# Performance work log

Hardware: AMD Instinct MI355X
Metric: run time of the kernel (lower is better)

The kernel has to match this reference:

```python
import jax, jax.numpy as jnp
import numpy as np

D_IN = 1024
D_OUT = 1024
NUM_HEADS = 16
HEAD_DIM = D_OUT // NUM_HEADS
CONTEXT_LEN = 2048


def setup_inputs() -> dict:
    key = jax.random.key(0)
    ks = jax.random.split(key, 7)
    scale = 0.02
    x = jax.random.normal(ks[0], (2, 2048, D_IN), dtype=jnp.float32)
    Wq = jax.random.normal(ks[1], (D_IN, D_OUT), dtype=jnp.float32) * scale
    bq = jnp.zeros((D_OUT,), dtype=jnp.float32)
    Wk = jax.random.normal(ks[2], (D_IN, D_OUT), dtype=jnp.float32) * scale
    bk = jnp.zeros((D_OUT,), dtype=jnp.float32)
    Wv = jax.random.normal(ks[3], (D_IN, D_OUT), dtype=jnp.float32) * scale
    bv = jnp.zeros((D_OUT,), dtype=jnp.float32)
    return {"x": x, "Wq": Wq, "bq": bq, "Wk": Wk, "bk": bk, "Wv": Wv, "bv": bv}


def reference(x, Wq, bq, Wk, bk, Wv, bv):
    B, S, _ = x.shape
    # QKV projections with bias
    q = x @ Wq + bq  # [B,S,D_OUT]
    k = x @ Wk + bk
    v = x @ Wv + bv
    # split heads -> [B,H,S,Dh]
    def heads(t):
        return t.reshape(B, S, NUM_HEADS, HEAD_DIM).transpose(0, 2, 1, 3)
    q, k, v = heads(q), heads(k), heads(v)
    # raw scores, then additive causal mask (-1e9 on strictly upper triangle),
    # then scale by 1/sqrt(head_dim) AFTER adding mask (matches original code)
    scores = jnp.einsum("bhqd,bhkd->bhqk", q, k)
    causal = jnp.tril(jnp.ones((S, S), dtype=bool))
    add_mask = jnp.where(causal, 0.0, -1e9).astype(scores.dtype)
    scores = scores + add_mask
    weights = jax.nn.softmax(scores / jnp.sqrt(jnp.asarray(HEAD_DIM, scores.dtype)), axis=-1)
    ctx = jnp.einsum("bhqk,bhkd->bhqd", weights, v)  # [B,H,S,Dh]
    return ctx.transpose(0, 2, 1, 3).reshape(B, S, D_OUT)
```

## Files before the change

### kernel.cpp

```cpp
#include <hip/hip_runtime.h>
#include <hip/hip_bf16.h>
#include <stdint.h>

#define D_IN 1024
#define NH 16
#define DH 64
#define SEQ 2048
#define BATCH 2

typedef unsigned short u16;
typedef __attribute__((ext_vector_type(8))) short short8;
typedef __attribute__((ext_vector_type(4))) float f32x4;

#define CSCALE 0.1803368801f

__device__ __forceinline__ u16 f2bf(float f) {
    union { float f; uint32_t u; } v; v.f = f;
    uint32_t r = v.u + 0x7FFF + ((v.u >> 16) & 1);
    return (u16)(r >> 16);
}

__device__ __forceinline__ float bf2f(u16 u) {
    union { uint32_t u; float f; } v; v.u = (uint32_t)u << 16;
    return v.f;
}

__device__ __forceinline__ uint32_t pktrunc(float a, float b) {
    union { float f; uint32_t u; } x, y;
    x.f = a; y.f = b;
    return __builtin_amdgcn_perm(y.u, x.u, 0x07060302u);
}

__device__ __forceinline__ void async16(const u16* g, u16* l) {
    __builtin_amdgcn_global_load_lds(
        (const __attribute__((address_space(1))) void*)g,
        (__attribute__((address_space(3))) void*)l, 16, 0, 0);
}

__global__ __launch_bounds__(256) void prep_kernel(
    const float* __restrict__ x, const float* __restrict__ Wq,
    const float* __restrict__ Wk, const float* __restrict__ Wv,
    u16* __restrict__ xb, u16* __restrict__ WT)
{
    __shared__ float tile[64][65];
    if (blockIdx.x < 4096) {
        int i = (blockIdx.x * 256 + threadIdx.x) * 4;
        float4 v = *(const float4*)(x + i);
        union { u16 u[4]; uint2 d; } o;
        o.u[0] = f2bf(v.x); o.u[1] = f2bf(v.y); o.u[2] = f2bf(v.z); o.u[3] = f2bf(v.w);
        *(uint2*)(xb + i) = o.d;
        return;
    }
    int idx = blockIdx.x - 4096;
    int mat = idx >> 8, rem = idx & 255;
    int k0 = (rem & 15) * 64, n0 = (rem >> 4) * 64;
    const float* W = (mat == 0) ? Wq : (mat == 1 ? Wk : Wv);
    int c = threadIdx.x & 63, rb = threadIdx.x >> 6;
    #pragma unroll
    for (int p = 0; p < 16; ++p) {
        int r = p * 4 + rb;
        tile[r][c] = W[(size_t)(k0 + r) * 1024 + n0 + c];
    }
    __syncthreads();
    #pragma unroll
    for (int p = 0; p < 16; ++p) {
        int r = p * 4 + rb;
        WT[((size_t)mat * 1024 + n0 + r) * 1024 + k0 + c] = f2bf(tile[c][r]);
    }
}

__global__ __launch_bounds__(512, 2) void qkv_gemm_kernel(
    const u16* __restrict__ xb, const u16* __restrict__ WT,
    const float* __restrict__ bq, const float* __restrict__ bk,
    const float* __restrict__ bv,
    u16* __restrict__ Qb, u16* __restrict__ Kb, u16* __restrict__ Vt)
{
    __shared__ u16 smem[65536];
    u16* As = smem;
    u16* Bs = smem + 32768;

    const int tid  = threadIdx.x;
    const int wave = tid >> 6, lane = tid & 63;
    const int quad = lane >> 4, l15 = lane & 15;
    const int wm = wave >> 2, wn = wave & 3;
    const int fsig = l15 & 7;

    const int lin = blockIdx.x;
    const int logical = (lin & 7) * 24 + (lin >> 3);
    const int by = logical / 12;
    const int bx = logical % 12;
    const int m0 = by * 256;
    const int n0 = bx * 256;

    const int ch  = tid & 7;
    const int rwT = tid >> 3;

    f32x4 acc[8][4];
    #pragma unroll
    for (int i = 0; i < 8; ++i)
        #pragma unroll
        for (int j = 0; j < 4; ++j)
            acc[i][j] = (f32x4){0.f, 0.f, 0.f, 0.f};

    auto stageA = [&](int buf, int kst) {
        #pragma unroll
        for (int r = 0; r < 4; ++r) {
            int row = r * 64 + rwT;
            int g = ch ^ (row & 7);
            async16(xb + (size_t)(m0 + row) * 1024 + kst + g * 8,
                    As + buf * 16384 + row * 64 + ch * 8);
        }
    };
    auto stageBh = [&](int buf, int kst, int half) {
        #pragma unroll
        for (int r = 0; r < 2; ++r) {
            int row = half * 128 + r * 64 + rwT;
            int g = ch ^ (row & 7);
            async16(WT + (size_t)(n0 + row) * 1024 + kst + g * 8,
                    Bs + buf * 16384 + row * 64 + ch * 8);
        }
    };

    stageA(0, 0);  stageBh(0, 0, 0);  stageBh(0, 0, 1);
    stageA(1, 64); stageBh(1, 64, 0); stageBh(1, 64, 1);
    asm volatile("s_waitcnt vmcnt(8)" ::: "memory");
    __builtin_amdgcn_sched_barrier(0);
    __builtin_amdgcn_s_barrier();

    for (int t = 0; t < 16; ++t) {
        const int cur = t & 1;
        const u16* Ab = As + cur * 16384;
        const u16* Bb = Bs + cur * 16384;
        const bool st = (t + 2 < 16);
        const int k2 = (t + 2) * 64;

        short8 bfr[4][2];
        #pragma unroll
        for (int j = 0; j < 4; ++j)
            #pragma unroll
            for (int kk = 0; kk < 2; ++kk)
                bfr[j][kk] = *(const short8*)(Bb + (wn * 64 + j * 16 + l15) * 64 +
                                              (((kk << 2) + quad) ^ fsig) * 8);

        #pragma unroll
        for (int p = 0; p < 4; ++p) {
            short8 af[2][2];
            #pragma unroll
            for (int i2 = 0; i2 < 2; ++i2)
                #pragma unroll
                for (int kk = 0; kk < 2; ++kk)
                    af[i2][kk] = *(const short8*)(Ab + (wm * 128 + (p * 2 + i2) * 16 + l15) * 64 +
                                                  (((kk << 2) + quad) ^ fsig) * 8);
            if (p == 1 && st) stageBh(cur, k2, 0);
            if (p == 2 && st) stageBh(cur, k2, 1);
            __builtin_amdgcn_s_barrier();
            if (p == 3 && st) stageA(cur, k2);
            __builtin_amdgcn_s_setprio(1);
            #pragma unroll
            for (int kk = 0; kk < 2; ++kk)
                #pragma unroll
                for (int i2 = 0; i2 < 2; ++i2)
                    #pragma unroll
                    for (int j = 0; j < 4; ++j)
                        acc[p * 2 + i2][j] = __builtin_amdgcn_mfma_f32_16x16x32_bf16(
                            af[i2][kk], bfr[j][kk], acc[p * 2 + i2][j], 0, 0, 0);
            __builtin_amdgcn_s_setprio(0);
            if (p == 3) {
                if (st)            { asm volatile("s_waitcnt vmcnt(8)" ::: "memory"); }
                else if (t == 14)  { asm volatile("s_waitcnt vmcnt(0)" ::: "memory"); }
                __builtin_amdgcn_sched_barrier(0);
            }
            __builtin_amdgcn_s_barrier();
        }
    }
    __syncthreads();

    const int mat = n0 >> 10;
    const int ncb = (n0 & 1023) + wn * 64;
    const int hh = ncb >> 6;
    const int bb = m0 >> 11, sb = m0 & 2047;

    if (mat < 2) {
        const float* bias = (mat == 0) ? bq : bk;
        u16* dst = (mat == 0) ? Qb : Kb;
        const float sc = (mat == 0) ? CSCALE : 1.0f;
        #pragma unroll
        for (int i = 0; i < 8; ++i) {
            int ss = sb + wm * 128 + i * 16 + quad * 4;
            #pragma unroll
            for (int j = 0; j < 4; ++j) {
                int dh = j * 16 + l15;
                float bval = bias[ncb + dh];
                size_t base = (((size_t)bb * NH + hh) * SEQ + ss) * DH + dh;
                #pragma unroll
                for (int r = 0; r < 4; ++r)
                    dst[base + (size_t)r * DH] = f2bf((acc[i][j][r] + bval) * sc);
            }
        }
    } else {
        u16* vt = smem + wave * (64 * 72);
        u16* vdst = Vt + ((size_t)(bb * NH + hh) * DH) * SEQ;
        #pragma unroll
        for (int h2 = 0; h2 < 2; ++h2) {
            #pragma unroll
            for (int i = 0; i < 4; ++i)
                #pragma unroll
                for (int j = 0; j < 4; ++j) {
                    float bval = bv[ncb + j * 16 + l15];
                    union { u16 u[4]; uint2 d; } o;
                    #pragma unroll
                    for (int r = 0; r < 4; ++r)
                        o.u[r] = f2bf(acc[h2 * 4 + i][j][r] + bval);
                    *(uint2*)(vt + (j * 16 + l15) * 72 + i * 16 + quad * 4) = o.d;
                }
            const int s0w = sb + wm * 128 + h2 * 64;
            #pragma unroll
            for (int it = 0; it < 8; ++it) {
                int dh = it * 8 + (lane >> 3);
                short8 v = *(const short8*)(vt + dh * 72 + (lane & 7) * 8);
                *(short8*)(vdst + (size_t)dh * SEQ + s0w + (lane & 7) * 8) = v;
            }
        }
    }
}

__device__ __forceinline__ void stage64(const u16* g0, size_t gstride, u16* lds,
                                        int wave, int lane)
{
    #pragma unroll
    for (int rnd = 0; rnd < 2; ++rnd) {
        int row = rnd * 32 + wave * 8 + (lane >> 3);
        int sig = ((row >> 3) & 1) * 4 + (row & 3);
        int c = (lane & 7) ^ sig;
        async16(g0 + (size_t)row * gstride + c * 8, lds + row * 64 + (lane & 7) * 8);
    }
}

__global__ __launch_bounds__(256) void flash_mfma_kernel(
    const u16* __restrict__ Qb, const u16* __restrict__ Kb,
    const u16* __restrict__ Vt, float* __restrict__ out,
    u16* __restrict__ Opart, float* __restrict__ Lpart)
{
    static const int JQT[24] = {7,15,15,14,14, 6,13,13,12,12, 5,11,11,10,10,
                                4, 9, 9, 8, 8, 3, 2, 1, 0};
    static const int JHF[24] = {-1,0,1,0,1, -1,0,1,0,1, -1,0,1,0,1,
                                -1,0,1,0,1, -1,-1,-1,-1};

    __shared__ u16 Ks[2][64 * 64];
    __shared__ u16 Vs[2][64 * 64];

    const int tid  = threadIdx.x;
    const int wave = tid >> 6, lane = tid & 63;
    const int quad = lane >> 4, l15 = lane & 15;
    const int bhx = blockIdx.x;
    const int b = bhx >> 4, h = bhx & 15;
    const int job = blockIdx.y;
    const int qt = JQT[job], hf = JHF[job];
    const int t0 = (hf == 1) ? qt + 1 : 0;
    const int t1 = (hf == 0) ? qt + 1 : 2 * qt + 2;
    const int q0 = qt * 128;
    const int wq0 = wave * 32;
    const size_t bh = (size_t)bhx;
    const u16* Qp = Qb + bh * SEQ * DH;
    const u16* Kp = Kb + bh * SEQ * DH;
    const u16* Vp = Vt + bh * DH * SEQ;

    short8 qf[2][2];
    #pragma unroll
    for (int qa = 0; qa < 2; ++qa) {
        const u16* qrp = Qp + (size_t)(q0 + wq0 + qa * 16 + l15) * DH;
        qf[qa][0] = *(const short8*)(qrp + quad * 8);
        qf[qa][1] = *(const short8*)(qrp + 32 + quad * 8);
    }

    const short8 ones = (short8){0x3F80, 0x3F80, 0x3F80, 0x3F80,
                                 0x3F80, 0x3F80, 0x3F80, 0x3F80};

    f32x4 O[2][4], L[2];
    #pragma unroll
    for (int pa = 0; pa < 2; ++pa) {
        #pragma unroll
        for (int f = 0; f < 4; ++f) O[pa][f] = (f32x4){0.f, 0.f, 0.f, 0.f};
        L[pa] = (f32x4){0.f, 0.f, 0.f, 0.f};
    }

    const int wqmax = q0 + wq0 + 31;
    const int krbase = (l15 >> 2) * 8 + (l15 & 3);
    const int ksig   = ((l15 >> 2) & 1) * 4 + (l15 & 3);
    const int vsig   = ((l15 >> 3) & 1) * 4 + (l15 & 3);

    stage64(Kp + (size_t)t0 * 64 * DH, DH, Ks[t0 & 1], wave, lane);
    stage64(Vp + t0 * 64, SEQ, Vs[t0 & 1], wave, lane);
    __syncthreads();

    for (int t = t0; t < t1; ++t) {
        const int cur = t & 1;
        if (t + 1 < t1) {
            int k1 = (t + 1) * 64;
            stage64(Kp + (size_t)k1 * DH, DH, Ks[cur ^ 1], wave, lane);
            stage64(Vp + k1, SEQ, Vs[cur ^ 1], wave, lane);
        }
        const int k0 = t * 64;
        if (k0 <= wqmax) {
            f32x4 sf[4][2];
            #pragma unroll
            for (int fj = 0; fj < 4; ++fj) {
                int krow = (fj >> 1) * 32 + krbase + (fj & 1) * 4;
                const u16* kp = &Ks[cur][krow * 64];
                short8 k0f = *(const short8*)(kp + (quad ^ ksig) * 8);
                short8 k1f = *(const short8*)(kp + ((4 + quad) ^ ksig) * 8);
                #pragma unroll
                for (int qa = 0; qa < 2; ++qa) {
                    f32x4 s = (f32x4){0.f, 0.f, 0.f, 0.f};
                    s = __builtin_amdgcn_mfma_f32_16x16x32_bf16(k0f, qf[qa][0], s, 0, 0, 0);
                    s = __builtin_amdgcn_mfma_f32_16x16x32_bf16(k1f, qf[qa][1], s, 0, 0, 0);
                    sf[fj][qa] = s;
                }
            }
            const bool diag = (k0 + 63 > q0 + wq0);
            short8 pA[2][2];
            #pragma unroll
            for (int qa = 0; qa < 2; ++qa) {
                #pragma unroll
                for (int fj = 0; fj < 4; ++fj)
                    #pragma unroll
                    for (int r = 0; r < 4; ++r) {
                        float p = __builtin_amdgcn_exp2f(sf[fj][qa][r]);
                        if (diag) {
                            int key = k0 + (fj >> 1) * 32 + quad * 8 + (fj & 1) * 4 + r;
                            int qg  = q0 + wq0 + qa * 16 + l15;
                            p = (key <= qg) ? p : 0.f;
                        }
                        sf[fj][qa][r] = p;
                    }
                union { uint32_t d[4]; short8 v; } a0, a1;
                a0.d[0] = pktrunc(sf[0][qa][0], sf[0][qa][1]);
                a0.d[1] = pktrunc(sf[0][qa][2], sf[0][qa][3]);
                a0.d[2] = pktrunc(sf[1][qa][0], sf[1][qa][1]);
                a0.d[3] = pktrunc(sf[1][qa][2], sf[1][qa][3]);
                a1.d[0] = pktrunc(sf[2][qa][0], sf[2][qa][1]);
                a1.d[1] = pktrunc(sf[2][qa][2], sf[2][qa][3]);
                a1.d[2] = pktrunc(sf[3][qa][0], sf[3][qa][1]);
                a1.d[3] = pktrunc(sf[3][qa][2], sf[3][qa][3]);
                pA[qa][0] = a0.v;
                pA[qa][1] = a1.v;
                L[qa] = __builtin_amdgcn_mfma_f32_16x16x32_bf16(pA[qa][0], ones, L[qa], 0, 0, 0);
                L[qa] = __builtin_amdgcn_mfma_f32_16x16x32_bf16(pA[qa][1], ones, L[qa], 0, 0, 0);
            }
            #pragma unroll
            for (int fo = 0; fo < 4; ++fo) {
                const u16* vrow = &Vs[cur][(fo * 16 + l15) * 64];
                short8 vb0 = *(const short8*)(vrow + (quad ^ vsig) * 8);
                short8 vb1 = *(const short8*)(vrow + ((4 + quad) ^ vsig) * 8);
                #pragma unroll
                for (int pa = 0; pa < 2; ++pa) {
                    O[pa][fo] = __builtin_amdgcn_mfma_f32_16x16x32_bf16(pA[pa][0], vb0, O[pa][fo], 0, 0, 0);
                    O[pa][fo] = __builtin_amdgcn_mfma_f32_16x16x32_bf16(pA[pa][1], vb1, O[pa][fo], 0, 0, 0);
                }
            }
        }
        __syncthreads();
    }

    if (hf < 0) {
        #pragma unroll
        for (int pa = 0; pa < 2; ++pa)
            #pragma unroll
            for (int fo = 0; fo < 4; ++fo)
                #pragma unroll
                for (int r = 0; r < 4; ++r) {
                    int s = q0 + wq0 + pa * 16 + quad * 4 + r;
                    out[((size_t)b * SEQ + s) * 1024 + h * DH + fo * 16 + l15] =
                        O[pa][fo][r] / L[pa][r];
                }
    } else {
        const int pi = (qt - 8) * 2 + hf;
        u16* op = Opart + (((size_t)pi * 32 + bhx) * 128) * 64;
        float* lp = Lpart + ((size_t)pi * 32 + bhx) * 128;
        #pragma unroll
        for (int pa = 0; pa < 2; ++pa) {
            #pragma unroll
            for (int fo = 0; fo < 4; ++fo)
                #pragma unroll
                for (int r = 0; r < 4; ++r) {
                    int ql = wq0 + pa * 16 + quad * 4 + r;
                    op[(size_t)ql * 64 + fo * 16 + l15] = f2bf(O[pa][fo][r]);
                }
            if (l15 == 0) {
                #pragma unroll
                for (int r = 0; r < 4; ++r)
                    lp[wq0 + pa * 16 + quad * 4 + r] = L[pa][r];
            }
        }
    }
}

__global__ __launch_bounds__(256) void combine_kernel(
    const u16* __restrict__ Opart, const float* __restrict__ Lpart,
    float* __restrict__ out)
{
    int blk = blockIdx.x;
    int qt = 8 + (blk >> 5);
    int bh = blk & 31;
    int b = bh >> 4, h = bh & 15;
    int pi0 = (qt - 8) * 2, pi1 = pi0 + 1;
    int tid = threadIdx.x;
    int q = tid >> 1, seg = (tid & 1) * 32;
    const u16* o0 = Opart + (((size_t)pi0 * 32 + bh) * 128 + q) * 64 + seg;
    const u16* o1 = Opart + (((size_t)pi1 * 32 + bh) * 128 + q) * 64 + seg;
    float inv = 1.0f / (Lpart[((size_t)pi0 * 32 + bh) * 128 + q] +
                        Lpart[((size_t)pi1 * 32 + bh) * 128 + q]);
    float* op = out + ((size_t)b * SEQ + qt * 128 + q) * 1024 + h * DH + seg;
    #pragma unroll
    for (int d = 0; d < 32; d += 4) {
        union { uint2 d2; u16 u[4]; } a, c;
        a.d2 = *(const uint2*)(o0 + d);
        c.d2 = *(const uint2*)(o1 + d);
        float4 v;
        v.x = (bf2f(a.u[0]) + bf2f(c.u[0])) * inv;
        v.y = (bf2f(a.u[1]) + bf2f(c.u[1])) * inv;
        v.z = (bf2f(a.u[2]) + bf2f(c.u[2])) * inv;
        v.w = (bf2f(a.u[3]) + bf2f(c.u[3])) * inv;
        *(float4*)(op + d) = v;
    }
}

extern "C" void kernel_launch(void* const* d_in, const int* in_sizes, int n_in,
                              void* d_out, int out_size, void* d_ws, size_t ws_size,
                              hipStream_t stream) {
    const float* x  = (const float*)d_in[0];
    const float* Wq = (const float*)d_in[1];
    const float* bq = (const float*)d_in[2];
    const float* Wk = (const float*)d_in[3];
    const float* bk = (const float*)d_in[4];
    const float* Wv = (const float*)d_in[5];
    const float* bv = (const float*)d_in[6];
    float* out = (float*)d_out;

    const size_t NX = (size_t)BATCH * SEQ * D_IN;
    const size_t NW = (size_t)3 * D_IN * 1024;
    const size_t NP = (size_t)BATCH * NH * SEQ * DH;
    u16* xb = (u16*)d_ws;
    u16* WT = xb + NX;
    u16* Qb = WT + NW;
    u16* Kb = Qb + NP;
    u16* Vt = Kb + NP;
    u16* Opart = xb;
    float* Lpart = (float*)(xb + NX);

    prep_kernel<<<4096 + 768, 256, 0, stream>>>(x, Wq, Wk, Wv, xb, WT);
    qkv_gemm_kernel<<<dim3(192), 512, 0, stream>>>(xb, WT, bq, bk, bv, Qb, Kb, Vt);
    flash_mfma_kernel<<<dim3(32, 24), 256, 0, stream>>>(Qb, Kb, Vt, out, Opart, Lpart);
    combine_kernel<<<256, 256, 0, stream>>>(Opart, Lpart, out);
}
```

Baseline: 156.2 us.

## Fuse split-KV combine into flash kernel via atomic counter; add setprio around MFMA

Measured after the change: 261.6 us. +67.5%, slower.

```diff
diff --git a/kernel.cpp b/kernel.cpp
--- a/kernel.cpp
+++ b/kernel.cpp
@@ -40,9 +40,13 @@
 __global__ __launch_bounds__(256) void prep_kernel(
     const float* __restrict__ x, const float* __restrict__ Wq,
     const float* __restrict__ Wk, const float* __restrict__ Wv,
-    u16* __restrict__ xb, u16* __restrict__ WT)
+    u16* __restrict__ xb, u16* __restrict__ WT, unsigned int* __restrict__ cnt)
 {
     __shared__ float tile[64][65];
+    if (blockIdx.x >= 4864) {
+        if (threadIdx.x < 256) cnt[threadIdx.x] = 0u;
+        return;
+    }
     if (blockIdx.x < 4096) {
         int i = (blockIdx.x * 256 + threadIdx.x) * 4;
         float4 v = *(const float4*)(x + i);
@@ -111,6 +115,15 @@
                     As + buf * 16384 + row * 64 + ch * 8);
         }
     };
+    auto stageAh = [&](int buf, int kst, int sel) {
+        #pragma unroll
+        for (int r = 0; r < 2; ++r) {
+            int row = (r * 2 + sel) * 64 + rwT;
+            int g = ch ^ (row & 7);
+            async16(xb + (size_t)(m0 + row) * 1024 + kst + g * 8,
+                    As + buf * 16384 + row * 64 + ch * 8);
+        }
+    };
     auto stageBh = [&](int buf, int kst, int half) {
         #pragma unroll
         for (int r = 0; r < 2; ++r) {
@@ -154,7 +167,8 @@
             if (p == 1 && st) stageBh(cur, k2, 0);
             if (p == 2 && st) stageBh(cur, k2, 1);
             __builtin_amdgcn_s_barrier();
-            if (p == 3 && st) stageA(cur, k2);
+            if (p == 2 && st) stageAh(cur, k2, 0);
+            if (p == 3 && st) stageAh(cur, k2, 1);
             __builtin_amdgcn_s_setprio(1);
             #pragma unroll
             for (int kk = 0; kk < 2; ++kk)
@@ -239,7 +253,8 @@
 __global__ __launch_bounds__(256) void flash_mfma_kernel(
     const u16* __restrict__ Qb, const u16* __restrict__ Kb,
     const u16* __restrict__ Vt, float* __restrict__ out,
-    u16* __restrict__ Opart, float* __restrict__ Lpart)
+    u16* __restrict__ Opart, float* __restrict__ Lpart,
+    unsigned int* __restrict__ cnt)
 {
     static const int JQT[24] = {7,15,15,14,14, 6,13,13,12,12, 5,11,11,10,10,
                                 4, 9, 9, 8, 8, 3, 2, 1, 0};
@@ -248,6 +263,7 @@
 
     __shared__ u16 Ks[2][64 * 64];
     __shared__ u16 Vs[2][64 * 64];
+    __shared__ unsigned int oldsh;
 
     const int tid  = threadIdx.x;
     const int wave = tid >> 6, lane = tid & 63;
@@ -303,6 +319,7 @@
         const int k0 = t * 64;
         if (k0 <= wqmax) {
             f32x4 sf[4][2];
+            __builtin_amdgcn_s_setprio(1);
             #pragma unroll
             for (int fj = 0; fj < 4; ++fj) {
                 int krow = (fj >> 1) * 32 + krbase + (fj & 1) * 4;
@@ -317,6 +334,7 @@
                     sf[fj][qa] = s;
                 }
             }
+            __builtin_amdgcn_s_setprio(0);
             const bool diag = (k0 + 63 > q0 + wq0);
             short8 pA[2][2];
             #pragma unroll
@@ -347,6 +365,7 @@
                 L[qa] = __builtin_amdgcn_mfma_f32_16x16x32_bf16(pA[qa][0], ones, L[qa], 0, 0, 0);
                 L[qa] = __builtin_amdgcn_mfma_f32_16x16x32_bf16(pA[qa][1], ones, L[qa], 0, 0, 0);
             }
+            __builtin_amdgcn_s_setprio(1);
             #pragma unroll
             for (int fo = 0; fo < 4; ++fo) {
                 const u16* vrow = &Vs[cur][(fo * 16 + l15) * 64];
@@ -358,6 +377,7 @@
                     O[pa][fo] = __builtin_amdgcn_mfma_f32_16x16x32_bf16(pA[pa][1], vb1, O[pa][fo], 0, 0, 0);
                 }
             }
+            __builtin_amdgcn_s_setprio(0);
         }
         __syncthreads();
     }
@@ -373,55 +393,53 @@
                     out[((size_t)b * SEQ + s) * 1024 + h * DH + fo * 16 + l15] =
                         O[pa][fo][r] / L[pa][r];
                 }
-    } else {
-        const int pi = (qt - 8) * 2 + hf;
-        u16* op = Opart + (((size_t)pi * 32 + bhx) * 128) * 64;
-        float* lp = Lpart + ((size_t)pi * 32 + bhx) * 128;
-        #pragma unroll
-        for (int pa = 0; pa < 2; ++pa) {
-            #pragma unroll
-            for (int fo = 0; fo < 4; ++fo)
-                #pragma unroll
-                for (int r = 0; r < 4; ++r) {
-                    int ql = wq0 + pa * 16 + quad * 4 + r;
-                    op[(size_t)ql * 64 + fo * 16 + l15] = f2bf(O[pa][fo][r]);
-                }
-            if (l15 == 0) {
-                #pragma unroll
-                for (int r = 0; r < 4; ++r)
-                    lp[wq0 + pa * 16 + quad * 4 + r] = L[pa][r];
-            }
-        }
-    }
-}
-
-__global__ __launch_bounds__(256) void combine_kernel(
-    const u16* __restrict__ Opart, const float* __restrict__ Lpart,
-    float* __restrict__ out)
-{
-    int blk = blockIdx.x;
-    int qt = 8 + (blk >> 5);
-    int bh = blk & 31;
-    int b = bh >> 4, h = bh & 15;
-    int pi0 = (qt - 8) * 2, pi1 = pi0 + 1;
-    int tid = threadIdx.x;
-    int q = tid >> 1, seg = (tid & 1) * 32;
-    const u16* o0 = Opart + (((size_t)pi0 * 32 + bh) * 128 + q) * 64 + seg;
-    const u16* o1 = Opart + (((size_t)pi1 * 32 + bh) * 128 + q) * 64 + seg;
-    float inv = 1.0f / (Lpart[((size_t)pi0 * 32 + bh) * 128 + q] +
-                        Lpart[((size_t)pi1 * 32 + bh) * 128 + q]);
-    float* op = out + ((size_t)b * SEQ + qt * 128 + q) * 1024 + h * DH + seg;
-    #pragma unroll
-    for (int d = 0; d < 32; d += 4) {
-        union { uint2 d2; u16 u[4]; } a, c;
-        a.d2 = *(const uint2*)(o0 + d);
-        c.d2 = *(const uint2*)(o1 + d);
-        float4 v;
-        v.x = (bf2f(a.u[0]) + bf2f(c.u[0])) * inv;
-        v.y = (bf2f(a.u[1]) + bf2f(c.u[1])) * inv;
-        v.z = (bf2f(a.u[2]) + bf2f(c.u[2])) * inv;
-        v.w = (bf2f(a.u[3]) + bf2f(c.u[3])) * inv;
-        *(float4*)(op + d) = v;
+        return;
+    }
+
+    const int pi = (qt - 8) * 2 + hf;
+    u16* op = Opart + (((size_t)pi * 32 + bhx) * 128) * 64;
+    float* lp = Lpart + ((size_t)pi * 32 + bhx) * 128;
+    #pragma unroll
+    for (int pa = 0; pa < 2; ++pa) {
+        #pragma unroll
+        for (int fo = 0; fo < 4; ++fo)
+            #pragma unroll
+            for (int r = 0; r < 4; ++r) {
+                int ql = wq0 + pa * 16 + quad * 4 + r;
+                op[(size_t)ql * 64 + fo * 16 + l15] = f2bf(O[pa][fo][r]);
+            }
+        if (l15 == 0) {
+            #pragma unroll
+            for (int r = 0; r < 4; ++r)
+                lp[wq0 + pa * 16 + quad * 4 + r] = L[pa][r];
+        }
+    }
+
+    __threadfence();
+    __syncthreads();
+    if (tid == 0) oldsh = atomicAdd(&cnt[(qt - 8) * 32 + bhx], 1u);
+    __syncthreads();
+    if (oldsh == 1) {
+        __threadfence();
+        const int pi0 = (qt - 8) * 2, pi1 = pi0 + 1;
+        int q = tid >> 1, seg = (tid & 1) * 32;
+        const u16* o0 = Opart + (((size_t)pi0 * 32 + bhx) * 128 + q) * 64 + seg;
+        const u16* o1 = Opart + (((size_t)pi1 * 32 + bhx) * 128 + q) * 64 + seg;
+        float inv = 1.0f / (Lpart[((size_t)pi0 * 32 + bhx) * 128 + q] +
+                            Lpart[((size_t)pi1 * 32 + bhx) * 128 + q]);
+        float* opf = out + ((size_t)b * SEQ + q0 + q) * 1024 + h * DH + seg;
+        #pragma unroll
+        for (int d = 0; d < 32; d += 4) {
+            union { uint2 d2; u16 u[4]; } a, c;
+            a.d2 = *(const uint2*)(o0 + d);
+            c.d2 = *(const uint2*)(o1 + d);
+            float4 v;
+            v.x = (bf2f(a.u[0]) + bf2f(c.u[0])) * inv;
+            v.y = (bf2f(a.u[1]) + bf2f(c.u[1])) * inv;
+            v.z = (bf2f(a.u[2]) + bf2f(c.u[2])) * inv;
+            v.w = (bf2f(a.u[3]) + bf2f(c.u[3])) * inv;
+            *(float4*)(opf + d) = v;
+        }
     }
 }
 
@@ -447,9 +465,9 @@
     u16* Vt = Kb + NP;
     u16* Opart = xb;
     float* Lpart = (float*)(xb + NX);
-
-    prep_kernel<<<4096 + 768, 256, 0, stream>>>(x, Wq, Wk, Wv, xb, WT);
+    unsigned int* cnt = (unsigned int*)(Vt + NP);
+
+    prep_kernel<<<4865, 256, 0, stream>>>(x, Wq, Wk, Wv, xb, WT, cnt);
     qkv_gemm_kernel<<<dim3(192), 512, 0, stream>>>(xb, WT, bq, bk, bv, Qb, Kb, Vt);
-    flash_mfma_kernel<<<dim3(32, 24), 256, 0, stream>>>(Qb, Kb, Vt, out, Opart, Lpart);
-    combine_kernel<<<256, 256, 0, stream>>>(Opart, Lpart, out);
-}
+    flash_mfma_kernel<<<dim3(32, 24), 256, 0, stream>>>(Qb, Kb, Vt, out, Opart, Lpart, cnt);
+}
```

## Triple-buffer K/V tiles with fine-grained vmcnt waits and MFMA priority hints

Applied to the files above, without the earlier changes.

Result: no change. 156.2 us (-0.0%).

```diff
diff --git a/kernel.cpp b/kernel.cpp
--- a/kernel.cpp
+++ b/kernel.cpp
@@ -246,8 +246,8 @@
     static const int JHF[24] = {-1,0,1,0,1, -1,0,1,0,1, -1,0,1,0,1,
                                 -1,0,1,0,1, -1,-1,-1,-1};
 
-    __shared__ u16 Ks[2][64 * 64];
-    __shared__ u16 Vs[2][64 * 64];
+    __shared__ u16 Ks[3][64 * 64];
+    __shared__ u16 Vs[3][64 * 64];
 
     const int tid  = threadIdx.x;
     const int wave = tid >> 6, lane = tid & 63;
@@ -289,20 +289,32 @@
     const int ksig   = ((l15 >> 2) & 1) * 4 + (l15 & 3);
     const int vsig   = ((l15 >> 3) & 1) * 4 + (l15 & 3);
 
-    stage64(Kp + (size_t)t0 * 64 * DH, DH, Ks[t0 & 1], wave, lane);
-    stage64(Vp + t0 * 64, SEQ, Vs[t0 & 1], wave, lane);
-    __syncthreads();
+    int cur = t0 % 3;
+    stage64(Kp + (size_t)t0 * 64 * DH, DH, Ks[cur], wave, lane);
+    stage64(Vp + t0 * 64, SEQ, Vs[cur], wave, lane);
+    if (t0 + 1 < t1) {
+        int nb = cur + 1; if (nb >= 3) nb -= 3;
+        stage64(Kp + (size_t)(t0 + 1) * 64 * DH, DH, Ks[nb], wave, lane);
+        stage64(Vp + (t0 + 1) * 64, SEQ, Vs[nb], wave, lane);
+        asm volatile("s_waitcnt vmcnt(4)" ::: "memory");
+    } else {
+        asm volatile("s_waitcnt vmcnt(0)" ::: "memory");
+    }
+    __builtin_amdgcn_sched_barrier(0);
+    __builtin_amdgcn_s_barrier();
 
     for (int t = t0; t < t1; ++t) {
-        const int cur = t & 1;
-        if (t + 1 < t1) {
-            int k1 = (t + 1) * 64;
-            stage64(Kp + (size_t)k1 * DH, DH, Ks[cur ^ 1], wave, lane);
-            stage64(Vp + k1, SEQ, Vs[cur ^ 1], wave, lane);
+        const bool st = (t + 2 < t1);
+        if (st) {
+            int s2 = cur + 2; if (s2 >= 3) s2 -= 3;
+            int k2 = (t + 2) * 64;
+            stage64(Kp + (size_t)k2 * DH, DH, Ks[s2], wave, lane);
+            stage64(Vp + k2, SEQ, Vs[s2], wave, lane);
         }
         const int k0 = t * 64;
         if (k0 <= wqmax) {
             f32x4 sf[4][2];
+            __builtin_amdgcn_s_setprio(1);
             #pragma unroll
             for (int fj = 0; fj < 4; ++fj) {
                 int krow = (fj >> 1) * 32 + krbase + (fj & 1) * 4;
@@ -317,6 +329,7 @@
                     sf[fj][qa] = s;
                 }
             }
+            __builtin_amdgcn_s_setprio(0);
             const bool diag = (k0 + 63 > q0 + wq0);
             short8 pA[2][2];
             #pragma unroll
@@ -347,6 +360,7 @@
                 L[qa] = __builtin_amdgcn_mfma_f32_16x16x32_bf16(pA[qa][0], ones, L[qa], 0, 0, 0);
                 L[qa] = __builtin_amdgcn_mfma_f32_16x16x32_bf16(pA[qa][1], ones, L[qa], 0, 0, 0);
             }
+            __builtin_amdgcn_s_setprio(1);
             #pragma unroll
             for (int fo = 0; fo < 4; ++fo) {
                 const u16* vrow = &Vs[cur][(fo * 16 + l15) * 64];
@@ -358,8 +372,15 @@
                     O[pa][fo] = __builtin_amdgcn_mfma_f32_16x16x32_bf16(pA[pa][1], vb1, O[pa][fo], 0, 0, 0);
                 }
             }
-        }
-        __syncthreads();
+            __builtin_amdgcn_s_setprio(0);
+        }
+        if (t + 1 < t1) {
+            if (st) { asm volatile("s_waitcnt vmcnt(4)" ::: "memory"); }
+            else    { asm volatile("s_waitcnt vmcnt(0)" ::: "memory"); }
+            __builtin_amdgcn_sched_barrier(0);
+            __builtin_amdgcn_s_barrier();
+        }
+        cur = (cur + 1 >= 3) ? 0 : cur + 1;
     }
 
     if (hf < 0) {
```

## Split flash attention into fixed 8-tile KV chunks with uniform combine pass

Applied to the files above, without the earlier changes.

Measured after the change: 159.3 us. About the same (+2.0%).

```diff
diff --git a/kernel.cpp b/kernel.cpp
--- a/kernel.cpp
+++ b/kernel.cpp
@@ -238,13 +238,15 @@
 
 __global__ __launch_bounds__(256) void flash_mfma_kernel(
     const u16* __restrict__ Qb, const u16* __restrict__ Kb,
-    const u16* __restrict__ Vt, float* __restrict__ out,
+    const u16* __restrict__ Vt,
     u16* __restrict__ Opart, float* __restrict__ Lpart)
 {
-    static const int JQT[24] = {7,15,15,14,14, 6,13,13,12,12, 5,11,11,10,10,
-                                4, 9, 9, 8, 8, 3, 2, 1, 0};
-    static const int JHF[24] = {-1,0,1,0,1, -1,0,1,0,1, -1,0,1,0,1,
-                                -1,0,1,0,1, -1,-1,-1,-1};
+    static const int JQ[40] = {15,15,15,15,14,14,14,13,13,13,12,12,12,11,11,11,
+                               10,10, 9, 9, 8, 8, 7, 7, 6, 5, 4, 3,
+                               14,10, 6, 2,13, 9, 5, 1,12, 8, 4, 0};
+    static const int JC[40] = { 0, 1, 2, 3, 0, 1, 2, 0, 1, 2, 0, 1, 2, 0, 1, 2,
+                                0, 1, 0, 1, 0, 1, 0, 1, 0, 0, 0, 0,
+                                3, 2, 1, 0, 3, 2, 1, 0, 3, 2, 1, 0};
 
     __shared__ u16 Ks[2][64 * 64];
     __shared__ u16 Vs[2][64 * 64];
@@ -253,11 +255,10 @@
     const int wave = tid >> 6, lane = tid & 63;
     const int quad = lane >> 4, l15 = lane & 15;
     const int bhx = blockIdx.x;
-    const int b = bhx >> 4, h = bhx & 15;
     const int job = blockIdx.y;
-    const int qt = JQT[job], hf = JHF[job];
-    const int t0 = (hf == 1) ? qt + 1 : 0;
-    const int t1 = (hf == 0) ? qt + 1 : 2 * qt + 2;
+    const int qt = JQ[job], cc = JC[job];
+    const int ta = cc * 8;
+    const int tb = min(ta + 8, 2 * qt + 2);
     const int q0 = qt * 128;
     const int wq0 = wave * 32;
     const size_t bh = (size_t)bhx;
@@ -289,13 +290,13 @@
     const int ksig   = ((l15 >> 2) & 1) * 4 + (l15 & 3);
     const int vsig   = ((l15 >> 3) & 1) * 4 + (l15 & 3);
 
-    stage64(Kp + (size_t)t0 * 64 * DH, DH, Ks[t0 & 1], wave, lane);
-    stage64(Vp + t0 * 64, SEQ, Vs[t0 & 1], wave, lane);
+    stage64(Kp + (size_t)ta * 64 * DH, DH, Ks[0], wave, lane);
+    stage64(Vp + ta * 64, SEQ, Vs[0], wave, lane);
     __syncthreads();
 
-    for (int t = t0; t < t1; ++t) {
+    for (int t = ta; t < tb; ++t) {
         const int cur = t & 1;
-        if (t + 1 < t1) {
+        if (t + 1 < tb) {
             int k1 = (t + 1) * 64;
             stage64(Kp + (size_t)k1 * DH, DH, Ks[cur ^ 1], wave, lane);
             stage64(Vp + k1, SEQ, Vs[cur ^ 1], wave, lane);
@@ -303,6 +304,7 @@
         const int k0 = t * 64;
         if (k0 <= wqmax) {
             f32x4 sf[4][2];
+            __builtin_amdgcn_s_setprio(1);
             #pragma unroll
             for (int fj = 0; fj < 4; ++fj) {
                 int krow = (fj >> 1) * 32 + krbase + (fj & 1) * 4;
@@ -317,6 +319,7 @@
                     sf[fj][qa] = s;
                 }
             }
+            __builtin_amdgcn_s_setprio(0);
             const bool diag = (k0 + 63 > q0 + wq0);
             short8 pA[2][2];
             #pragma unroll
@@ -347,6 +350,7 @@
                 L[qa] = __builtin_amdgcn_mfma_f32_16x16x32_bf16(pA[qa][0], ones, L[qa], 0, 0, 0);
                 L[qa] = __builtin_amdgcn_mfma_f32_16x16x32_bf16(pA[qa][1], ones, L[qa], 0, 0, 0);
             }
+            __builtin_amdgcn_s_setprio(1);
             #pragma unroll
             for (int fo = 0; fo < 4; ++fo) {
                 const u16* vrow = &Vs[cur][(fo * 16 + l15) * 64];
@@ -358,39 +362,27 @@
                     O[pa][fo] = __builtin_amdgcn_mfma_f32_16x16x32_bf16(pA[pa][1], vb1, O[pa][fo], 0, 0, 0);
                 }
             }
+            __builtin_amdgcn_s_setprio(0);
         }
         __syncthreads();
     }
 
-    if (hf < 0) {
-        #pragma unroll
-        for (int pa = 0; pa < 2; ++pa)
-            #pragma unroll
-            for (int fo = 0; fo < 4; ++fo)
-                #pragma unroll
-                for (int r = 0; r < 4; ++r) {
-                    int s = q0 + wq0 + pa * 16 + quad * 4 + r;
-                    out[((size_t)b * SEQ + s) * 1024 + h * DH + fo * 16 + l15] =
-                        O[pa][fo][r] / L[pa][r];
-                }
-    } else {
-        const int pi = (qt - 8) * 2 + hf;
-        u16* op = Opart + (((size_t)pi * 32 + bhx) * 128) * 64;
-        float* lp = Lpart + ((size_t)pi * 32 + bhx) * 128;
-        #pragma unroll
-        for (int pa = 0; pa < 2; ++pa) {
-            #pragma unroll
-            for (int fo = 0; fo < 4; ++fo)
-                #pragma unroll
-                for (int r = 0; r < 4; ++r) {
-                    int ql = wq0 + pa * 16 + quad * 4 + r;
-                    op[(size_t)ql * 64 + fo * 16 + l15] = f2bf(O[pa][fo][r]);
-                }
-            if (l15 == 0) {
-                #pragma unroll
-                for (int r = 0; r < 4; ++r)
-                    lp[wq0 + pa * 16 + quad * 4 + r] = L[pa][r];
-            }
+    const int slot = ((qt << 2) + cc) * 32 + bhx;
+    u16* op = Opart + (size_t)slot * (128 * 64);
+    float* lp = Lpart + (size_t)slot * 128;
+    #pragma unroll
+    for (int pa = 0; pa < 2; ++pa) {
+        #pragma unroll
+        for (int fo = 0; fo < 4; ++fo)
+            #pragma unroll
+            for (int r = 0; r < 4; ++r) {
+                int ql = wq0 + pa * 16 + quad * 4 + r;
+                op[(size_t)ql * 64 + fo * 16 + l15] = f2bf(O[pa][fo][r]);
+            }
+        if (l15 == 0) {
+            #pragma unroll
+            for (int r = 0; r < 4; ++r)
+                lp[wq0 + pa * 16 + quad * 4 + r] = L[pa][r];
         }
     }
 }
@@ -400,27 +392,42 @@
     float* __restrict__ out)
 {
     int blk = blockIdx.x;
-    int qt = 8 + (blk >> 5);
+    int qt = blk >> 5;
     int bh = blk & 31;
     int b = bh >> 4, h = bh & 15;
-    int pi0 = (qt - 8) * 2, pi1 = pi0 + 1;
+    int nch = (2 * qt + 9) >> 3;
     int tid = threadIdx.x;
     int q = tid >> 1, seg = (tid & 1) * 32;
-    const u16* o0 = Opart + (((size_t)pi0 * 32 + bh) * 128 + q) * 64 + seg;
-    const u16* o1 = Opart + (((size_t)pi1 * 32 + bh) * 128 + q) * 64 + seg;
-    float inv = 1.0f / (Lpart[((size_t)pi0 * 32 + bh) * 128 + q] +
-                        Lpart[((size_t)pi1 * 32 + bh) * 128 + q]);
+
+    float l = 0.f;
+    for (int c = 0; c < nch; ++c)
+        l += Lpart[((size_t)((qt << 2) + c) * 32 + bh) * 128 + q];
+    float inv = 1.0f / l;
+
+    float acc[32];
+    #pragma unroll
+    for (int d = 0; d < 32; ++d) acc[d] = 0.f;
+    for (int c = 0; c < nch; ++c) {
+        const u16* o = Opart + (((size_t)((qt << 2) + c) * 32 + bh) * 128 + q) * 64 + seg;
+        #pragma unroll
+        for (int d = 0; d < 32; d += 4) {
+            union { uint2 d2; u16 u[4]; } a;
+            a.d2 = *(const uint2*)(o + d);
+            acc[d]     += bf2f(a.u[0]);
+            acc[d + 1] += bf2f(a.u[1]);
+            acc[d + 2] += bf2f(a.u[2]);
+            acc[d + 3] += bf2f(a.u[3]);
+        }
+    }
+
     float* op = out + ((size_t)b * SEQ + qt * 128 + q) * 1024 + h * DH + seg;
     #pragma unroll
     for (int d = 0; d < 32; d += 4) {
-        union { uint2 d2; u16 u[4]; } a, c;
-        a.d2 = *(const uint2*)(o0 + d);
-        c.d2 = *(const uint2*)(o1 + d);
         float4 v;
-        v.x = (bf2f(a.u[0]) + bf2f(c.u[0])) * inv;
-        v.y = (bf2f(a.u[1]) + bf2f(c.u[1])) * inv;
-        v.z = (bf2f(a.u[2]) + bf2f(c.u[2])) * inv;
-        v.w = (bf2f(a.u[3]) + bf2f(c.u[3])) * inv;
+        v.x = acc[d] * inv;
+        v.y = acc[d + 1] * inv;
+        v.z = acc[d + 2] * inv;
+        v.w = acc[d + 3] * inv;
         *(float4*)(op + d) = v;
     }
 }
@@ -445,11 +452,11 @@
     u16* Qb = WT + NW;
     u16* Kb = Qb + NP;
     u16* Vt = Kb + NP;
-    u16* Opart = xb;
-    float* Lpart = (float*)(xb + NX);
+    u16* Opart = Vt + NP;
+    float* Lpart = (float*)(Opart + (size_t)2048 * 128 * 64);
 
     prep_kernel<<<4096 + 768, 256, 0, stream>>>(x, Wq, Wk, Wv, xb, WT);
     qkv_gemm_kernel<<<dim3(192), 512, 0, stream>>>(xb, WT, bq, bk, bv, Qb, Kb, Vt);
-    flash_mfma_kernel<<<dim3(32, 24), 256, 0, stream>>>(Qb, Kb, Vt, out, Opart, Lpart);
-    combine_kernel<<<256, 256, 0, stream>>>(Opart, Lpart, out);
-}
+    flash_mfma_kernel<<<dim3(32, 40), 256, 0, stream>>>(Qb, Kb, Vt, Opart, Lpart);
+    combine_kernel<<<512, 256, 0, stream>>>(Opart, Lpart, out);
+}
```
